# Kernel tuning notes

Measured on AMD Instinct MI355X. Metric: run time of the kernel, lower is better.

The kernel has to match this reference:

```python
import jax, jax.numpy as jnp
import numpy as np

NUM_HEADS = 8
HEAD_DIM = 16
HIDDEN = 128  # NUM_HEADS * HEAD_DIM
EPS = 1e-12
NEG_BIG = -1000000.0


def setup_inputs() -> dict:
    key = jax.random.key(0)
    ks = jax.random.split(key, 12)
    bz, n, na, hid = 16, 1024, 32, HIDDEN
    std = 0.02
    return {
        "h": jax.random.normal(ks[0], (bz, n, hid), dtype=jnp.float32),
        "message": jax.random.normal(ks[1], (bz, n, na, hid), dtype=jnp.float32),
        "mask": jax.random.randint(ks[2], (bz, n, na, 1), 0, 2).astype(jnp.float32),
        "qW": jax.random.normal(ks[3], (hid, hid), dtype=jnp.float32) * std,
        "qb": jnp.zeros((hid,), jnp.float32),
        "kW": jax.random.normal(ks[4], (hid, hid), dtype=jnp.float32) * std,
        "kb": jnp.zeros((hid,), jnp.float32),
        "vW": jax.random.normal(ks[5], (hid, hid), dtype=jnp.float32) * std,
        "vb": jnp.zeros((hid,), jnp.float32),
        "dW": jax.random.normal(ks[6], (hid, hid), dtype=jnp.float32) * std,
        "db": jnp.zeros((hid,), jnp.float32),
        "ln_w": jnp.ones((hid,), jnp.float32),
        "ln_b": jnp.zeros((hid,), jnp.float32),
    }


def _layernorm(x, w, b):
    u = jnp.mean(x, axis=-1, keepdims=True)
    s = jnp.mean((x - u) ** 2, axis=-1, keepdims=True)
    return w * ((x - u) / jnp.sqrt(s + EPS)) + b


def reference(h, message, mask, qW, qb, kW, kb, vW, vb, dW, db, ln_w, ln_b):
    bz, n, na, hid = message.shape
    # projections (torch Linear math: x @ W^T + b; here weights stored as [in,out])
    q = h @ qW + qb                              # [b,n,hid]
    k = message @ kW + kb                        # [b,n,na,hid]
    v = jax.nn.relu(message @ vW + vb)           # [b,n,na,hid]
    # split heads
    qh = q.reshape(bz, n, NUM_HEADS, HEAD_DIM)                 # [b,n,h,d] (q_len=1)
    kh = k.reshape(bz, n, na, NUM_HEADS, HEAD_DIM)             # [b,n,k,h,d]
    vh = v.reshape(bz, n, na, NUM_HEADS, HEAD_DIM)
    m = mask[..., 0][:, :, None, :]                            # [b,n,1,k] broadcast over heads
    scores = jnp.einsum("bnhd,bnkhd->bnhk", qh, kh)
    scores = scores / jnp.sqrt(jnp.asarray(HEAD_DIM, scores.dtype)) * m
    scores = jnp.where(scores == 0.0, NEG_BIG, scores)
    probs = jax.nn.softmax(scores, axis=-1) * m                # [b,n,h,k]
    ctx = jnp.einsum("bnhk,bnkhd->bnhd", probs, vh).reshape(bz, n, hid)
    hidden_states = ctx @ dW + db
    return _layernorm(hidden_states + h, ln_w, ln_b)
```

## Files before the change

### kernel.cpp

```cpp
#include <hip/hip_runtime.h>

typedef short  bf16x8 __attribute__((ext_vector_type(8)));
typedef float  f32x4  __attribute__((ext_vector_type(4)));

#define NA   32
#define HID  128
#define TPB  8
#define KSTR 136

__device__ __forceinline__ unsigned short f2bf(float f) {
  unsigned int u = __float_as_uint(f);
  return (unsigned short)((u + 0x7FFFu + ((u >> 16) & 1u)) >> 16);
}
__device__ __forceinline__ float bf2f(unsigned short s) {
  return __uint_as_float(((unsigned int)s) << 16);
}
__device__ __forceinline__ void barrier_lds() {
  asm volatile("s_waitcnt lgkmcnt(0)" ::: "memory");
  __builtin_amdgcn_s_barrier();
  asm volatile("" ::: "memory");
}

__global__ __launch_bounds__(256, 2) void soft_attn_v6(
    const float* __restrict__ h, const float* __restrict__ msg,
    const float* __restrict__ mask,
    const float* __restrict__ qW, const float* __restrict__ qb,
    const float* __restrict__ kW, const float* __restrict__ kb,
    const float* __restrict__ vW, const float* __restrict__ vb,
    const float* __restrict__ dW, const float* __restrict__ db,
    const float* __restrict__ lnw, const float* __restrict__ lnb,
    float* __restrict__ out)
{
  const int t    = threadIdx.x;
  const int lane = t & 63;
  const int w    = t >> 6;
  const int lm   = lane & 15;
  const int lg   = lane >> 4;
  const int n0   = w * 32;
  const int tok0 = blockIdx.x * TPB;

  __shared__ __align__(16) short          s_msgF[2][8 * 64 * 8];
  __shared__ __align__(16) unsigned short s_k[NA * KSTR];
  __shared__ __align__(16) unsigned short s_v[NA * KSTR];
  __shared__ __align__(16) float          s_qall[TPB * HID];
  __shared__ __align__(16) float          s_p[8 * NA];
  __shared__ __align__(16) short          s_ctxF[4 * 64 * 8];
  __shared__ __align__(16) char           s_un[4096];
  short* s_hF   = (short*)s_un;
  float* s_dall = (float*)s_un;

  f32x4 P[2][2][2];
#pragma unroll
  for (int d = 0; d < 2; ++d)
#pragma unroll
    for (int j = 0; j < 2; ++j) {
      const int f = j * 4 + w, mt = f >> 2, ks = f & 3;
      const float* mp = msg + (size_t)(tok0 + d) * (NA * HID) + (mt * 16 + lm) * HID + ks * 32 + lg * 8;
      P[d][j][0] = *(const f32x4*)mp; P[d][j][1] = *(const f32x4*)(mp + 4);
    }

  float m8[TPB];
#pragma unroll
  for (int i = 0; i < TPB; ++i) m8[i] = mask[(size_t)(tok0 + i) * NA + (lane & 31)];

#pragma unroll
  for (int j = 0; j < 4; ++j) ((unsigned int*)s_ctxF)[t + 256 * j] = 0u;
  {
    bf16x8 sv;
#pragma unroll
    for (int e = 0; e < 8; ++e) sv[e] = 0;
    if (lm < TPB) {
      const float* hp = h + (size_t)(tok0 + lm) * HID + w * 32 + lg * 8;
      const f32x4 x0 = *(const f32x4*)hp;
      const f32x4 x1 = *(const f32x4*)(hp + 4);
#pragma unroll
      for (int e = 0; e < 4; ++e) { sv[e] = (short)f2bf(x0[e]); sv[4 + e] = (short)f2bf(x1[e]); }
    }
    ((bf16x8*)s_hF)[w * 64 + lane] = sv;
  }
  {
    bf16x8 Bq[2][4];
    float qb2[2];
#pragma unroll
    for (int nt = 0; nt < 2; ++nt) {
      const int col = n0 + nt * 16 + lm;
      qb2[nt] = qb[col];
#pragma unroll
      for (int ks = 0; ks < 4; ++ks) {
        bf16x8 bq;
#pragma unroll
        for (int e = 0; e < 8; ++e)
          bq[e] = (short)f2bf(qW[(size_t)(ks * 32 + lg * 8 + e) * HID + col]);
        Bq[nt][ks] = bq;
      }
    }
    __syncthreads();
    f32x4 accq[2];
#pragma unroll
    for (int nt = 0; nt < 2; ++nt) accq[nt] = (f32x4){qb2[nt], qb2[nt], qb2[nt], qb2[nt]};
#pragma unroll
    for (int ks = 0; ks < 4; ++ks) {
      const bf16x8 a = ((const bf16x8*)s_hF)[ks * 64 + lane];
#pragma unroll
      for (int nt = 0; nt < 2; ++nt)
        accq[nt] = __builtin_amdgcn_mfma_f32_16x16x32_bf16(a, Bq[nt][ks], accq[nt], 0, 0, 0);
    }
#pragma unroll
    for (int nt = 0; nt < 2; ++nt)
#pragma unroll
      for (int r = 0; r < 4; ++r) {
        const int row = lg * 4 + r;
        if (row < TPB) s_qall[row * HID + n0 + nt * 16 + lm] = accq[nt][r];
      }
  }

  bf16x8 Bk[2][4], Bv[2][4];
  float kb2[2], vb2[2];
#pragma unroll
  for (int nt = 0; nt < 2; ++nt) {
    const int col = n0 + nt * 16 + lm;
    kb2[nt] = kb[col]; vb2[nt] = vb[col];
#pragma unroll
    for (int ks = 0; ks < 4; ++ks) {
      bf16x8 bk, bv;
#pragma unroll
      for (int e = 0; e < 8; ++e) {
        const size_t r = (size_t)(ks * 32 + lg * 8 + e) * HID + col;
        bk[e] = (short)f2bf(kW[r]); bv[e] = (short)f2bf(vW[r]);
      }
      Bk[nt][ks] = bk; Bv[nt][ks] = bv;
    }
  }

#pragma unroll
  for (int it = 0; it < TPB; ++it) {
    const int tok = tok0 + it;
    const int buf = it & 1;

#pragma unroll
    for (int j = 0; j < 2; ++j) {
      const int f = j * 4 + w;
      bf16x8 sv;
#pragma unroll
      for (int e = 0; e < 4; ++e) {
        sv[e]     = (short)f2bf(P[buf][j][0][e]);
        sv[4 + e] = (short)f2bf(P[buf][j][1][e]);
      }
      ((bf16x8*)(&s_msgF[buf][0]))[f * 64 + lane] = sv;
    }

    if (it + 2 < TPB) {
#pragma unroll
      for (int j = 0; j < 2; ++j) {
        const int f = j * 4 + w, mt = f >> 2, ks = f & 3;
        const float* mp = msg + (size_t)(tok + 2) * (NA * HID) + (mt * 16 + lm) * HID + ks * 32 + lg * 8;
        P[buf][j][0] = *(const f32x4*)mp; P[buf][j][1] = *(const f32x4*)(mp + 4);
      }
    }
    barrier_lds();

    {
      f32x4 ak[2][2], av[2][2];
#pragma unroll
      for (int mt = 0; mt < 2; ++mt)
#pragma unroll
        for (int nt = 0; nt < 2; ++nt) {
          ak[mt][nt] = (f32x4){kb2[nt], kb2[nt], kb2[nt], kb2[nt]};
          av[mt][nt] = (f32x4){vb2[nt], vb2[nt], vb2[nt], vb2[nt]};
        }
#pragma unroll
      for (int ks = 0; ks < 4; ++ks) {
        const bf16x8 a0 = ((const bf16x8*)(&s_msgF[buf][0]))[ks * 64 + lane];
        const bf16x8 a1 = ((const bf16x8*)(&s_msgF[buf][0]))[(4 + ks) * 64 + lane];
#pragma unroll
        for (int nt = 0; nt < 2; ++nt) {
          ak[0][nt] = __builtin_amdgcn_mfma_f32_16x16x32_bf16(a0, Bk[nt][ks], ak[0][nt], 0, 0, 0);
          av[0][nt] = __builtin_amdgcn_mfma_f32_16x16x32_bf16(a0, Bv[nt][ks], av[0][nt], 0, 0, 0);
          ak[1][nt] = __builtin_amdgcn_mfma_f32_16x16x32_bf16(a1, Bk[nt][ks], ak[1][nt], 0, 0, 0);
          av[1][nt] = __builtin_amdgcn_mfma_f32_16x16x32_bf16(a1, Bv[nt][ks], av[1][nt], 0, 0, 0);
        }
      }
#pragma unroll
      for (int mt = 0; mt < 2; ++mt)
#pragma unroll
        for (int nt = 0; nt < 2; ++nt) {
          const int col  = n0 + nt * 16 + lm;
          const int row0 = mt * 16 + lg * 4;
#pragma unroll
          for (int r = 0; r < 4; ++r) {
            s_k[(row0 + r) * KSTR + col] = f2bf(ak[mt][nt][r]);
            s_v[(row0 + r) * KSTR + col] = f2bf(fmaxf(av[mt][nt][r], 0.f));
          }
        }
    }

    {
      const int hh = lane >> 5, a = lane & 31;
      const int head = 2 * w + hh;
      const f32x4* qr = (const f32x4*)(s_qall + it * HID + head * 16);
      const bf16x8 k0 = *(const bf16x8*)&s_k[a * KSTR + head * 16];
      const bf16x8 k1 = *(const bf16x8*)&s_k[a * KSTR + head * 16 + 8];
      const f32x4 q0 = qr[0], q1 = qr[1], q2 = qr[2], q3 = qr[3];
      float sc = 0.f;
#pragma unroll
      for (int e = 0; e < 4; ++e) {
        sc = fmaf(q0[e], bf2f((unsigned short)k0[e]), sc);
        sc = fmaf(q1[e], bf2f((unsigned short)k0[4 + e]), sc);
        sc = fmaf(q2[e], bf2f((unsigned short)k1[e]), sc);
        sc = fmaf(q3[e], bf2f((unsigned short)k1[4 + e]), sc);
      }
      const float mk = m8[it];
      sc = sc * 0.25f * mk;
      if (sc == 0.0f) sc = -1000000.0f;
      float mx = sc;
#pragma unroll
      for (int off = 16; off; off >>= 1) mx = fmaxf(mx, __shfl_xor(mx, off));
      const float ex = __expf(sc - mx);
      float sm = ex;
#pragma unroll
      for (int off = 16; off; off >>= 1) sm += __shfl_xor(sm, off);
      s_p[head * NA + a] = ex / sm * mk;
    }

    {
      const int o = n0 + (lane >> 1), half = lane & 1;
      const int head = o >> 4;
      const float* pr = s_p + head * NA + half * 16;
      float ctx = 0.f;
#pragma unroll
      for (int i = 0; i < 16; ++i)
        ctx = fmaf(pr[i], bf2f(s_v[(half * 16 + i) * KSTR + o]), ctx);
      ctx += __shfl_xor(ctx, 1);
      if (half == 0) {
        ((unsigned short*)s_ctxF)[(((o >> 5) * 64) + ((o >> 3) & 3) * 16 + it) * 8 + (o & 7)] = f2bf(ctx);
      }
    }
  }
  __syncthreads();

  {
    bf16x8 Bd[2][4];
    float db2[2];
#pragma unroll
    for (int nt = 0; nt < 2; ++nt) {
      const int col = n0 + nt * 16 + lm;
      db2[nt] = db[col];
#pragma unroll
      for (int ks = 0; ks < 4; ++ks) {
        bf16x8 bd;
#pragma unroll
        for (int e = 0; e < 8; ++e)
          bd[e] = (short)f2bf(dW[(size_t)(ks * 32 + lg * 8 + e) * HID + col]);
        Bd[nt][ks] = bd;
      }
    }
    f32x4 accd[2];
#pragma unroll
    for (int nt = 0; nt < 2; ++nt) accd[nt] = (f32x4){db2[nt], db2[nt], db2[nt], db2[nt]};
#pragma unroll
    for (int ks = 0; ks < 4; ++ks) {
      const bf16x8 a = ((const bf16x8*)s_ctxF)[ks * 64 + lane];
#pragma unroll
      for (int nt = 0; nt < 2; ++nt)
        accd[nt] = __builtin_amdgcn_mfma_f32_16x16x32_bf16(a, Bd[nt][ks], accd[nt], 0, 0, 0);
    }
#pragma unroll
    for (int nt = 0; nt < 2; ++nt)
#pragma unroll
      for (int r = 0; r < 4; ++r) {
        const int row = lg * 4 + r;
        if (row < TPB) s_dall[row * HID + n0 + nt * 16 + lm] = accd[nt][r];
      }
  }
  __syncthreads();

  {
    const int row = t >> 5, seg = t & 31;
    const f32x4 xd = *(const f32x4*)(s_dall + row * HID + seg * 4);
    const f32x4 xh = *(const f32x4*)(h + (size_t)(tok0 + row) * HID + seg * 4);
    float x[4];
    float s1 = 0.f, s2 = 0.f;
#pragma unroll
    for (int e = 0; e < 4; ++e) { x[e] = xd[e] + xh[e]; s1 += x[e]; s2 += x[e] * x[e]; }
#pragma unroll
    for (int off = 16; off; off >>= 1) { s1 += __shfl_xor(s1, off); s2 += __shfl_xor(s2, off); }
    const float u   = s1 * (1.f / 128.f);
    const float var = s2 * (1.f / 128.f) - u * u;
    const float rs  = rsqrtf(var + 1e-12f);
    const f32x4 w4 = *(const f32x4*)(lnw + seg * 4);
    const f32x4 b4 = *(const f32x4*)(lnb + seg * 4);
    f32x4 y;
#pragma unroll
    for (int e = 0; e < 4; ++e) y[e] = w4[e] * ((x[e] - u) * rs) + b4[e];
    *(f32x4*)(out + (size_t)(tok0 + row) * HID + seg * 4) = y;
  }
}

extern "C" void kernel_launch(void* const* d_in, const int* in_sizes, int n_in,
                              void* d_out, int out_size, void* d_ws, size_t ws_size,
                              hipStream_t stream) {
  const float* h    = (const float*)d_in[0];
  const float* msg  = (const float*)d_in[1];
  const float* mask = (const float*)d_in[2];
  const float* qW   = (const float*)d_in[3];
  const float* qb   = (const float*)d_in[4];
  const float* kW   = (const float*)d_in[5];
  const float* kb   = (const float*)d_in[6];
  const float* vW   = (const float*)d_in[7];
  const float* vb   = (const float*)d_in[8];
  const float* dW   = (const float*)d_in[9];
  const float* db   = (const float*)d_in[10];
  const float* lnw  = (const float*)d_in[11];
  const float* lnb  = (const float*)d_in[12];
  float* out = (float*)d_out;

  const int n_tokens = in_sizes[0] / HID;
  const int nblocks  = n_tokens / TPB;
  soft_attn_v6<<<nblocks, 256, 0, stream>>>(
      h, msg, mask, qW, qb, kW, kb, vW, vb, dW, db, lnw, lnb, out);
}
```

Baseline: 140.9 us.

## Compute probs·V with MFMA using transposed V layout and vectorized K stores

```diff
diff --git a/kernel.cpp b/kernel.cpp
--- a/kernel.cpp
+++ b/kernel.cpp
@@ -1,12 +1,14 @@
 #include <hip/hip_runtime.h>
 
-typedef short  bf16x8 __attribute__((ext_vector_type(8)));
-typedef float  f32x4  __attribute__((ext_vector_type(4)));
+typedef short  bf16x8  __attribute__((ext_vector_type(8)));
+typedef short  short4v __attribute__((ext_vector_type(4)));
+typedef float  f32x4   __attribute__((ext_vector_type(4)));
 
 #define NA   32
 #define HID  128
 #define TPB  8
 #define KSTR 136
+#define VSTR 40
 
 __device__ __forceinline__ unsigned short f2bf(float f) {
   unsigned int u = __float_as_uint(f);
@@ -21,7 +23,7 @@
   asm volatile("" ::: "memory");
 }
 
-__global__ __launch_bounds__(256, 2) void soft_attn_v6(
+__global__ __launch_bounds__(256, 2) void soft_attn_v7(
     const float* __restrict__ h, const float* __restrict__ msg,
     const float* __restrict__ mask,
     const float* __restrict__ qW, const float* __restrict__ qb,
@@ -41,9 +43,9 @@
 
   __shared__ __align__(16) short          s_msgF[2][8 * 64 * 8];
   __shared__ __align__(16) unsigned short s_k[NA * KSTR];
-  __shared__ __align__(16) unsigned short s_v[NA * KSTR];
+  __shared__ __align__(16) unsigned short s_vT[HID * VSTR];
   __shared__ __align__(16) float          s_qall[TPB * HID];
-  __shared__ __align__(16) float          s_p[8 * NA];
+  __shared__ __align__(16) unsigned short s_pB[8 * NA];
   __shared__ __align__(16) short          s_ctxF[4 * 64 * 8];
   __shared__ __align__(16) char           s_un[4096];
   short* s_hF   = (short*)s_un;
@@ -58,7 +60,6 @@
       const float* mp = msg + (size_t)(tok0 + d) * (NA * HID) + (mt * 16 + lm) * HID + ks * 32 + lg * 8;
       P[d][j][0] = *(const f32x4*)mp; P[d][j][1] = *(const f32x4*)(mp + 4);
     }
-
   float m8[TPB];
 #pragma unroll
   for (int i = 0; i < TPB; ++i) m8[i] = mask[(size_t)(tok0 + i) * NA + (lane & 31)];
@@ -115,11 +116,13 @@
   }
 
   bf16x8 Bk[2][4], Bv[2][4];
-  float kb2[2], vb2[2];
+  f32x4 kb4[2];
+  float vb2[2];
 #pragma unroll
   for (int nt = 0; nt < 2; ++nt) {
     const int col = n0 + nt * 16 + lm;
-    kb2[nt] = kb[col]; vb2[nt] = vb[col];
+    kb4[nt] = *(const f32x4*)(kb + n0 + nt * 16 + lg * 4);
+    vb2[nt] = vb[col];
 #pragma unroll
     for (int ks = 0; ks < 4; ++ks) {
       bf16x8 bk, bv;
@@ -148,7 +151,6 @@
       }
       ((bf16x8*)(&s_msgF[buf][0]))[f * 64 + lane] = sv;
     }
-
     if (it + 2 < TPB) {
 #pragma unroll
       for (int j = 0; j < 2; ++j) {
@@ -160,37 +162,55 @@
     barrier_lds();
 
     {
-      f32x4 ak[2][2], av[2][2];
-#pragma unroll
-      for (int mt = 0; mt < 2; ++mt)
-#pragma unroll
-        for (int nt = 0; nt < 2; ++nt) {
-          ak[mt][nt] = (f32x4){kb2[nt], kb2[nt], kb2[nt], kb2[nt]};
-          av[mt][nt] = (f32x4){vb2[nt], vb2[nt], vb2[nt], vb2[nt]};
-        }
+      f32x4 ck[2][2];
+#pragma unroll
+      for (int nt = 0; nt < 2; ++nt)
+#pragma unroll
+        for (int mt = 0; mt < 2; ++mt) ck[nt][mt] = kb4[nt];
 #pragma unroll
       for (int ks = 0; ks < 4; ++ks) {
         const bf16x8 a0 = ((const bf16x8*)(&s_msgF[buf][0]))[ks * 64 + lane];
         const bf16x8 a1 = ((const bf16x8*)(&s_msgF[buf][0]))[(4 + ks) * 64 + lane];
 #pragma unroll
         for (int nt = 0; nt < 2; ++nt) {
-          ak[0][nt] = __builtin_amdgcn_mfma_f32_16x16x32_bf16(a0, Bk[nt][ks], ak[0][nt], 0, 0, 0);
-          av[0][nt] = __builtin_amdgcn_mfma_f32_16x16x32_bf16(a0, Bv[nt][ks], av[0][nt], 0, 0, 0);
-          ak[1][nt] = __builtin_amdgcn_mfma_f32_16x16x32_bf16(a1, Bk[nt][ks], ak[1][nt], 0, 0, 0);
-          av[1][nt] = __builtin_amdgcn_mfma_f32_16x16x32_bf16(a1, Bv[nt][ks], av[1][nt], 0, 0, 0);
+          ck[nt][0] = __builtin_amdgcn_mfma_f32_16x16x32_bf16(Bk[nt][ks], a0, ck[nt][0], 0, 0, 0);
+          ck[nt][1] = __builtin_amdgcn_mfma_f32_16x16x32_bf16(Bk[nt][ks], a1, ck[nt][1], 0, 0, 0);
         }
       }
 #pragma unroll
+      for (int nt = 0; nt < 2; ++nt)
+#pragma unroll
+        for (int mt = 0; mt < 2; ++mt) {
+          short4v kp;
+#pragma unroll
+          for (int r = 0; r < 4; ++r) kp[r] = (short)f2bf(ck[nt][mt][r]);
+          *(short4v*)&s_k[(mt * 16 + lm) * KSTR + n0 + nt * 16 + lg * 4] = kp;
+        }
+    }
+    {
+      f32x4 cv[2][2];
+#pragma unroll
       for (int mt = 0; mt < 2; ++mt)
 #pragma unroll
+        for (int nt = 0; nt < 2; ++nt) cv[mt][nt] = (f32x4){vb2[nt], vb2[nt], vb2[nt], vb2[nt]};
+#pragma unroll
+      for (int ks = 0; ks < 4; ++ks) {
+        const bf16x8 a0 = ((const bf16x8*)(&s_msgF[buf][0]))[ks * 64 + lane];
+        const bf16x8 a1 = ((const bf16x8*)(&s_msgF[buf][0]))[(4 + ks) * 64 + lane];
+#pragma unroll
         for (int nt = 0; nt < 2; ++nt) {
-          const int col  = n0 + nt * 16 + lm;
-          const int row0 = mt * 16 + lg * 4;
-#pragma unroll
-          for (int r = 0; r < 4; ++r) {
-            s_k[(row0 + r) * KSTR + col] = f2bf(ak[mt][nt][r]);
-            s_v[(row0 + r) * KSTR + col] = f2bf(fmaxf(av[mt][nt][r], 0.f));
-          }
+          cv[0][nt] = __builtin_amdgcn_mfma_f32_16x16x32_bf16(a0, Bv[nt][ks], cv[0][nt], 0, 0, 0);
+          cv[1][nt] = __builtin_amdgcn_mfma_f32_16x16x32_bf16(a1, Bv[nt][ks], cv[1][nt], 0, 0, 0);
+        }
+      }
+#pragma unroll
+      for (int mt = 0; mt < 2; ++mt)
+#pragma unroll
+        for (int nt = 0; nt < 2; ++nt) {
+          short4v vp;
+#pragma unroll
+          for (int r = 0; r < 4; ++r) vp[r] = (short)f2bf(fmaxf(cv[mt][nt][r], 0.f));
+          *(short4v*)&s_vT[(n0 + nt * 16 + lm) * VSTR + mt * 16 + lg * 4] = vp;
         }
     }
 
@@ -212,27 +232,22 @@
       const float mk = m8[it];
       sc = sc * 0.25f * mk;
       if (sc == 0.0f) sc = -1000000.0f;
-      float mx = sc;
-#pragma unroll
-      for (int off = 16; off; off >>= 1) mx = fmaxf(mx, __shfl_xor(mx, off));
-      const float ex = __expf(sc - mx);
+      const float ex = __expf(fmaxf(sc, -80.f));
       float sm = ex;
 #pragma unroll
       for (int off = 16; off; off >>= 1) sm += __shfl_xor(sm, off);
-      s_p[head * NA + a] = ex / sm * mk;
-    }
-
-    {
-      const int o = n0 + (lane >> 1), half = lane & 1;
-      const int head = o >> 4;
-      const float* pr = s_p + head * NA + half * 16;
-      float ctx = 0.f;
-#pragma unroll
-      for (int i = 0; i < 16; ++i)
-        ctx = fmaf(pr[i], bf2f(s_v[(half * 16 + i) * KSTR + o]), ctx);
-      ctx += __shfl_xor(ctx, 1);
-      if (half == 0) {
-        ((unsigned short*)s_ctxF)[(((o >> 5) * 64) + ((o >> 3) & 3) * 16 + it) * 8 + (o & 7)] = f2bf(ctx);
+      s_pB[head * NA + a] = f2bf(ex / sm * mk);
+    }
+
+#pragma unroll
+    for (int nt = 0; nt < 2; ++nt) {
+      const int head = 2 * w + nt;
+      const bf16x8 pa = *(const bf16x8*)&s_pB[head * NA + lg * 8];
+      const bf16x8 vf = *(const bf16x8*)&s_vT[(n0 + nt * 16 + lm) * VSTR + lg * 8];
+      const f32x4 pv = __builtin_amdgcn_mfma_f32_16x16x32_bf16(pa, vf, (f32x4){0.f, 0.f, 0.f, 0.f}, 0, 0, 0);
+      if (lg == 0) {
+        const int o = n0 + nt * 16 + lm;
+        ((unsigned short*)s_ctxF)[(((o >> 5) * 64) + ((o >> 3) & 3) * 16 + it) * 8 + (o & 7)] = f2bf(pv[0]);
       }
     }
   }
@@ -316,6 +331,6 @@
 
   const int n_tokens = in_sizes[0] / HID;
   const int nblocks  = n_tokens / TPB;
-  soft_attn_v6<<<nblocks, 256, 0, stream>>>(
+  soft_attn_v7<<<nblocks, 256, 0, stream>>>(
       h, msg, mask, qW, qb, kW, kb, vW, vb, dW, db, lnw, lnb, out);
 }
```

Measured after the change: 152.1 us. +7.9%, slower.

## Process token pairs per iteration and drop softmax max reduction

Applied to the files above, without the earlier changes.

```diff
diff --git a/kernel.cpp b/kernel.cpp
--- a/kernel.cpp
+++ b/kernel.cpp
@@ -21,7 +21,7 @@
   asm volatile("" ::: "memory");
 }
 
-__global__ __launch_bounds__(256, 2) void soft_attn_v6(
+__global__ __launch_bounds__(256, 2) void soft_attn_v8(
     const float* __restrict__ h, const float* __restrict__ msg,
     const float* __restrict__ mask,
     const float* __restrict__ qW, const float* __restrict__ qb,
@@ -39,11 +39,11 @@
   const int n0   = w * 32;
   const int tok0 = blockIdx.x * TPB;
 
-  __shared__ __align__(16) short          s_msgF[2][8 * 64 * 8];
-  __shared__ __align__(16) unsigned short s_k[NA * KSTR];
-  __shared__ __align__(16) unsigned short s_v[NA * KSTR];
+  __shared__ __align__(16) short          s_msgF[16 * 64 * 8];
+  __shared__ __align__(16) unsigned short s_k[2][NA * KSTR];
+  __shared__ __align__(16) unsigned short s_v[2][NA * KSTR];
   __shared__ __align__(16) float          s_qall[TPB * HID];
-  __shared__ __align__(16) float          s_p[8 * NA];
+  __shared__ __align__(16) float          s_p[2][8 * NA];
   __shared__ __align__(16) short          s_ctxF[4 * 64 * 8];
   __shared__ __align__(16) char           s_un[4096];
   short* s_hF   = (short*)s_un;
@@ -51,14 +51,13 @@
 
   f32x4 P[2][2][2];
 #pragma unroll
-  for (int d = 0; d < 2; ++d)
+  for (int tk = 0; tk < 2; ++tk)
 #pragma unroll
     for (int j = 0; j < 2; ++j) {
       const int f = j * 4 + w, mt = f >> 2, ks = f & 3;
-      const float* mp = msg + (size_t)(tok0 + d) * (NA * HID) + (mt * 16 + lm) * HID + ks * 32 + lg * 8;
-      P[d][j][0] = *(const f32x4*)mp; P[d][j][1] = *(const f32x4*)(mp + 4);
-    }
-
+      const float* mp = msg + (size_t)(tok0 + tk) * (NA * HID) + (mt * 16 + lm) * HID + ks * 32 + lg * 8;
+      P[tk][j][0] = *(const f32x4*)mp; P[tk][j][1] = *(const f32x4*)(mp + 4);
+    }
   float m8[TPB];
 #pragma unroll
   for (int i = 0; i < TPB; ++i) m8[i] = mask[(size_t)(tok0 + i) * NA + (lane & 31)];
@@ -133,51 +132,59 @@
   }
 
 #pragma unroll
-  for (int it = 0; it < TPB; ++it) {
-    const int tok = tok0 + it;
-    const int buf = it & 1;
-
-#pragma unroll
-    for (int j = 0; j < 2; ++j) {
-      const int f = j * 4 + w;
-      bf16x8 sv;
-#pragma unroll
-      for (int e = 0; e < 4; ++e) {
-        sv[e]     = (short)f2bf(P[buf][j][0][e]);
-        sv[4 + e] = (short)f2bf(P[buf][j][1][e]);
-      }
-      ((bf16x8*)(&s_msgF[buf][0]))[f * 64 + lane] = sv;
-    }
-
-    if (it + 2 < TPB) {
+  for (int pr = 0; pr < 4; ++pr) {
+#pragma unroll
+    for (int tk = 0; tk < 2; ++tk)
 #pragma unroll
       for (int j = 0; j < 2; ++j) {
-        const int f = j * 4 + w, mt = f >> 2, ks = f & 3;
-        const float* mp = msg + (size_t)(tok + 2) * (NA * HID) + (mt * 16 + lm) * HID + ks * 32 + lg * 8;
-        P[buf][j][0] = *(const f32x4*)mp; P[buf][j][1] = *(const f32x4*)(mp + 4);
-      }
+        const int f = j * 4 + w;
+        bf16x8 sv;
+#pragma unroll
+        for (int e = 0; e < 4; ++e) {
+          sv[e]     = (short)f2bf(P[tk][j][0][e]);
+          sv[4 + e] = (short)f2bf(P[tk][j][1][e]);
+        }
+        ((bf16x8*)s_msgF)[(tk * 8 + f) * 64 + lane] = sv;
+      }
+    if (pr + 1 < 4) {
+#pragma unroll
+      for (int tk = 0; tk < 2; ++tk)
+#pragma unroll
+        for (int j = 0; j < 2; ++j) {
+          const int f = j * 4 + w, mt = f >> 2, ks = f & 3;
+          const float* mp = msg + (size_t)(tok0 + 2 * (pr + 1) + tk) * (NA * HID) + (mt * 16 + lm) * HID + ks * 32 + lg * 8;
+          P[tk][j][0] = *(const f32x4*)mp; P[tk][j][1] = *(const f32x4*)(mp + 4);
+        }
     }
     barrier_lds();
 
     {
-      f32x4 ak[2][2], av[2][2];
+      f32x4 kA[2][2], kB[2][2], vA[2][2], vB[2][2];
 #pragma unroll
       for (int mt = 0; mt < 2; ++mt)
 #pragma unroll
         for (int nt = 0; nt < 2; ++nt) {
-          ak[mt][nt] = (f32x4){kb2[nt], kb2[nt], kb2[nt], kb2[nt]};
-          av[mt][nt] = (f32x4){vb2[nt], vb2[nt], vb2[nt], vb2[nt]};
+          kA[mt][nt] = (f32x4){kb2[nt], kb2[nt], kb2[nt], kb2[nt]};
+          kB[mt][nt] = kA[mt][nt];
+          vA[mt][nt] = (f32x4){vb2[nt], vb2[nt], vb2[nt], vb2[nt]};
+          vB[mt][nt] = vA[mt][nt];
         }
 #pragma unroll
       for (int ks = 0; ks < 4; ++ks) {
-        const bf16x8 a0 = ((const bf16x8*)(&s_msgF[buf][0]))[ks * 64 + lane];
-        const bf16x8 a1 = ((const bf16x8*)(&s_msgF[buf][0]))[(4 + ks) * 64 + lane];
+        const bf16x8 aA0 = ((const bf16x8*)s_msgF)[(0 + ks) * 64 + lane];
+        const bf16x8 aA1 = ((const bf16x8*)s_msgF)[(4 + ks) * 64 + lane];
+        const bf16x8 aB0 = ((const bf16x8*)s_msgF)[(8 + ks) * 64 + lane];
+        const bf16x8 aB1 = ((const bf16x8*)s_msgF)[(12 + ks) * 64 + lane];
 #pragma unroll
         for (int nt = 0; nt < 2; ++nt) {
-          ak[0][nt] = __builtin_amdgcn_mfma_f32_16x16x32_bf16(a0, Bk[nt][ks], ak[0][nt], 0, 0, 0);
-          av[0][nt] = __builtin_amdgcn_mfma_f32_16x16x32_bf16(a0, Bv[nt][ks], av[0][nt], 0, 0, 0);
-          ak[1][nt] = __builtin_amdgcn_mfma_f32_16x16x32_bf16(a1, Bk[nt][ks], ak[1][nt], 0, 0, 0);
-          av[1][nt] = __builtin_amdgcn_mfma_f32_16x16x32_bf16(a1, Bv[nt][ks], av[1][nt], 0, 0, 0);
+          kA[0][nt] = __builtin_amdgcn_mfma_f32_16x16x32_bf16(aA0, Bk[nt][ks], kA[0][nt], 0, 0, 0);
+          kB[0][nt] = __builtin_amdgcn_mfma_f32_16x16x32_bf16(aB0, Bk[nt][ks], kB[0][nt], 0, 0, 0);
+          kA[1][nt] = __builtin_amdgcn_mfma_f32_16x16x32_bf16(aA1, Bk[nt][ks], kA[1][nt], 0, 0, 0);
+          kB[1][nt] = __builtin_amdgcn_mfma_f32_16x16x32_bf16(aB1, Bk[nt][ks], kB[1][nt], 0, 0, 0);
+          vA[0][nt] = __builtin_amdgcn_mfma_f32_16x16x32_bf16(aA0, Bv[nt][ks], vA[0][nt], 0, 0, 0);
+          vB[0][nt] = __builtin_amdgcn_mfma_f32_16x16x32_bf16(aB0, Bv[nt][ks], vB[0][nt], 0, 0, 0);
+          vA[1][nt] = __builtin_amdgcn_mfma_f32_16x16x32_bf16(aA1, Bv[nt][ks], vA[1][nt], 0, 0, 0);
+          vB[1][nt] = __builtin_amdgcn_mfma_f32_16x16x32_bf16(aB1, Bv[nt][ks], vB[1][nt], 0, 0, 0);
         }
       }
 #pragma unroll
@@ -188,18 +195,23 @@
           const int row0 = mt * 16 + lg * 4;
 #pragma unroll
           for (int r = 0; r < 4; ++r) {
-            s_k[(row0 + r) * KSTR + col] = f2bf(ak[mt][nt][r]);
-            s_v[(row0 + r) * KSTR + col] = f2bf(fmaxf(av[mt][nt][r], 0.f));
+            s_k[0][(row0 + r) * KSTR + col] = f2bf(kA[mt][nt][r]);
+            s_k[1][(row0 + r) * KSTR + col] = f2bf(kB[mt][nt][r]);
+            s_v[0][(row0 + r) * KSTR + col] = f2bf(fmaxf(vA[mt][nt][r], 0.f));
+            s_v[1][(row0 + r) * KSTR + col] = f2bf(fmaxf(vB[mt][nt][r], 0.f));
           }
         }
     }
-
-    {
+    barrier_lds();
+
+#pragma unroll
+    for (int tk = 0; tk < 2; ++tk) {
+      const int it = 2 * pr + tk;
       const int hh = lane >> 5, a = lane & 31;
       const int head = 2 * w + hh;
       const f32x4* qr = (const f32x4*)(s_qall + it * HID + head * 16);
-      const bf16x8 k0 = *(const bf16x8*)&s_k[a * KSTR + head * 16];
-      const bf16x8 k1 = *(const bf16x8*)&s_k[a * KSTR + head * 16 + 8];
+      const bf16x8 k0 = *(const bf16x8*)&s_k[tk][a * KSTR + head * 16];
+      const bf16x8 k1 = *(const bf16x8*)&s_k[tk][a * KSTR + head * 16 + 8];
       const f32x4 q0 = qr[0], q1 = qr[1], q2 = qr[2], q3 = qr[3];
       float sc = 0.f;
 #pragma unroll
@@ -212,24 +224,23 @@
       const float mk = m8[it];
       sc = sc * 0.25f * mk;
       if (sc == 0.0f) sc = -1000000.0f;
-      float mx = sc;
-#pragma unroll
-      for (int off = 16; off; off >>= 1) mx = fmaxf(mx, __shfl_xor(mx, off));
-      const float ex = __expf(sc - mx);
+      const float ex = __expf(fmaxf(sc, -80.f));
       float sm = ex;
 #pragma unroll
       for (int off = 16; off; off >>= 1) sm += __shfl_xor(sm, off);
-      s_p[head * NA + a] = ex / sm * mk;
-    }
-
-    {
+      s_p[tk][head * NA + a] = ex / sm * mk;
+    }
+
+#pragma unroll
+    for (int tk = 0; tk < 2; ++tk) {
+      const int it = 2 * pr + tk;
       const int o = n0 + (lane >> 1), half = lane & 1;
       const int head = o >> 4;
-      const float* pr = s_p + head * NA + half * 16;
+      const float* pr_ = s_p[tk] + head * NA + half * 16;
       float ctx = 0.f;
 #pragma unroll
       for (int i = 0; i < 16; ++i)
-        ctx = fmaf(pr[i], bf2f(s_v[(half * 16 + i) * KSTR + o]), ctx);
+        ctx = fmaf(pr_[i], bf2f(s_v[tk][(half * 16 + i) * KSTR + o]), ctx);
       ctx += __shfl_xor(ctx, 1);
       if (half == 0) {
         ((unsigned short*)s_ctxF)[(((o >> 5) * 64) + ((o >> 3) & 3) * 16 + it) * 8 + (o & 7)] = f2bf(ctx);
@@ -316,6 +327,6 @@
 
   const int n_tokens = in_sizes[0] / HID;
   const int nblocks  = n_tokens / TPB;
-  soft_attn_v6<<<nblocks, 256, 0, stream>>>(
+  soft_attn_v8<<<nblocks, 256, 0, stream>>>(
       h, msg, mask, qW, qb, kW, kb, vW, vb, dW, db, lnw, lnb, out);
 }
```

Measured after the change: 180.9 us. 1.28x slower.
